# Optimization experiments

Measured on AMD Instinct MI355X. Metric: run time of the kernel, lower is better.

## Reference

```python
import jax, jax.numpy as jnp
import numpy as np

B, S, D = 8, 1024, 1152
H, HD = 16, 72  # num_heads, head_dim

def setup_inputs() -> dict:
    key = jax.random.key(0)
    ks = jax.random.split(key, 7)
    hidden_states = jax.random.normal(ks[0], (B, S, D), dtype=jnp.float32)
    cos = jax.random.uniform(ks[1], (S, HD), dtype=jnp.float32)
    sin = jax.random.uniform(ks[2], (S, HD), dtype=jnp.float32)
    qkv_w = jax.random.normal(ks[3], (3 * D, D), dtype=jnp.float32) * 0.02
    qkv_b = jnp.zeros((3 * D,), dtype=jnp.float32)
    proj_w = jax.random.normal(ks[4], (D, D), dtype=jnp.float32) * 0.02
    proj_b = jnp.zeros((D,), dtype=jnp.float32)
    return {"hidden_states": hidden_states, "cos": cos, "sin": sin,
            "qkv_w": qkv_w, "qkv_b": qkv_b, "proj_w": proj_w, "proj_b": proj_b}

def _rotate_half(x):
    x1, x2 = jnp.split(x, 2, axis=-1)
    return jnp.concatenate((-x2, x1), axis=-1)

def reference(hidden_states, cos, sin, qkv_w, qkv_b, proj_w, proj_b):
    b, s, d = hidden_states.shape
    # fused QKV projection
    qkv = hidden_states @ qkv_w.T + qkv_b            # [B,S,3D]
    qkv = qkv.reshape(b, s, 3, H, HD)
    qkv = jnp.transpose(qkv, (2, 0, 3, 1, 4))        # [3,B,H,S,HD]
    q, k, v = qkv[0], qkv[1], qkv[2]
    # rotary embedding, cos/sin broadcast [1,1,S,HD]
    c = cos[None, None, :, :]
    sn = sin[None, None, :, :]
    q = q * c + _rotate_half(q) * sn
    k = k * c + _rotate_half(k) * sn
    # SDPA
    scale = HD ** -0.5
    scores = jnp.einsum('bhqd,bhkd->bhqk', q, k) * scale
    probs = jax.nn.softmax(scores, axis=-1)
    attn = jnp.einsum('bhqk,bhkd->bhqd', probs, v)   # [B,H,S,HD]
    attn = jnp.transpose(attn, (0, 2, 1, 3)).reshape(b, s, d)
    return attn @ proj_w.T + proj_b
```

## Files before the change

### kernel.cpp

```cpp
#include <hip/hip_runtime.h>
#include <hip/hip_bf16.h>


typedef __attribute__((ext_vector_type(8))) short short8;
typedef __attribute__((ext_vector_type(4))) float f32x4;

__device__ __forceinline__ unsigned int f2bf(float f) {
    unsigned int u = __float_as_uint(f);
    return (u + 0x7FFFu + ((u >> 16) & 1u)) >> 16;
}

__device__ __forceinline__ void stout(float* C, size_t idx, float v) { C[idx] = v; }
__device__ __forceinline__ void stout(__hip_bfloat16* C, size_t idx, float v) {
    C[idx] = __float2bfloat16(v);
}

__device__ __forceinline__ void async_cp16(const void* g, void* l) {
    __builtin_amdgcn_global_load_lds((const __attribute__((address_space(1))) void*)g,
                                     (__attribute__((address_space(3))) void*)l, 16, 0, 0);
}

__global__ void f32_to_bf16_pair(
    const float* __restrict__ s0, unsigned short* __restrict__ d0, int n0_4,
    const float* __restrict__ s1, unsigned short* __restrict__ d1, int n1_4,
    unsigned short* __restrict__ dz, int nz_4)
{
    int i = blockIdx.x * 256 + threadIdx.x;
    if (i < n0_4) {
        float4 f = ((const float4*)s0)[i];
        ushort4 r;
        r.x = (unsigned short)f2bf(f.x);
        r.y = (unsigned short)f2bf(f.y);
        r.z = (unsigned short)f2bf(f.z);
        r.w = (unsigned short)f2bf(f.w);
        ((ushort4*)d0)[i] = r;
        return;
    }
    i -= n0_4;
    if (i < n1_4) {
        float4 f = ((const float4*)s1)[i];
        ushort4 r;
        r.x = (unsigned short)f2bf(f.x);
        r.y = (unsigned short)f2bf(f.y);
        r.z = (unsigned short)f2bf(f.z);
        r.w = (unsigned short)f2bf(f.w);
        ((ushort4*)d1)[i] = r;
        return;
    }
    i -= n1_4;
    if (i < nz_4) {
        ushort4 z; z.x = 0; z.y = 0; z.z = 0; z.w = 0;
        ((ushort4*)dz)[i] = z;
    }
}

template <int ISB, int H>
__device__ __forceinline__ void stage_ht(const unsigned short* __restrict__ g, int ldg,
                                         int k0, unsigned short* l, int w, int lane)
{
#pragma unroll
    for (int t = 0; t < 2; t++) {
        const int c  = w * 2 + t;
        const int r0 = ISB ? ((c >> 2) * 64 + H * 32 + (c & 3) * 8)
                           : ((c & 8) * 16 + H * 64 + (c & 7) * 8);
        const int rl = r0 + (lane >> 3);
        const int gg = (lane & 7) ^ (lane >> 3);
        async_cp16(g + (size_t)rl * ldg + k0 + gg * 8, l + r0 * 64);
    }
}

#define LDA(MH, SRC)                                                              \
    _Pragma("unroll") for (int mi = 0; mi < 4; ++mi) {                            \
        Af[mi][0] = *(const short8*)((SRC) + aRow + (MH) * 4096 + mi * 1024 + g0); \
        Af[mi][1] = *(const short8*)((SRC) + aRow + (MH) * 4096 + mi * 1024 + g1); \
    }

#define LDB(DST, NH, SRC)                                                         \
    _Pragma("unroll") for (int ni = 0; ni < 2; ++ni) {                            \
        DST[ni][0] = *(const short8*)((SRC) + bRow + (NH) * 2048 + ni * 1024 + g0); \
        DST[ni][1] = *(const short8*)((SRC) + bRow + (NH) * 2048 + ni * 1024 + g1); \
    }

#define MFMAS(MH, NH, PB)                                                         \
    __builtin_amdgcn_s_setprio(1);                                                \
    _Pragma("unroll") for (int mi = 0; mi < 4; ++mi)                              \
    _Pragma("unroll") for (int ni = 0; ni < 2; ++ni) {                            \
        acc[(MH) * 4 + mi][(NH) * 2 + ni] = __builtin_amdgcn_mfma_f32_16x16x32_bf16( \
            Af[mi][0], PB[ni][0], acc[(MH) * 4 + mi][(NH) * 2 + ni], 0, 0, 0);    \
        acc[(MH) * 4 + mi][(NH) * 2 + ni] = __builtin_amdgcn_mfma_f32_16x16x32_bf16( \
            Af[mi][1], PB[ni][1], acc[(MH) * 4 + mi][(NH) * 2 + ni], 0, 0, 0);    \
    }                                                                             \
    __builtin_amdgcn_s_setprio(0);

#define MIDBAR()                                                   \
    do {                                                           \
        __builtin_amdgcn_s_barrier();                              \
        asm volatile("s_waitcnt lgkmcnt(0)" ::: "memory");         \
        __builtin_amdgcn_sched_barrier(0);                         \
    } while (0)

#define ENDBAR()                                                   \
    do {                                                           \
        __builtin_amdgcn_s_barrier();                              \
        __builtin_amdgcn_sched_barrier(0);                         \
    } while (0)

template <typename OT>
__global__ __launch_bounds__(512, 2) void gemm_bt_256(
    const __hip_bfloat16* __restrict__ Abf,
    const __hip_bfloat16* __restrict__ Bbf,
    const float* __restrict__ bias,
    OT* __restrict__ C,
    int M, int Nreal, int K)
{
    __shared__ __align__(16) unsigned short smem[2][2][256 * 64];

    const int tid  = threadIdx.x;
    const int lane = tid & 63;
    const int w    = tid >> 6;
    const int wm   = w >> 2;
    const int wn   = w & 3;
    const int q    = lane >> 4;
    const int fr   = lane & 15;
    const int xr   = fr & 7;

    const int nwg = gridDim.x * gridDim.y;
    const int lin = blockIdx.y * gridDim.x + blockIdx.x;
    const int swz = (lin & 7) * (nwg >> 3) + (lin >> 3);
    const int bn  = (swz % gridDim.x) * 256;
    const int bm  = (swz / gridDim.x) * 256;

    const unsigned short* Ag = (const unsigned short*)Abf + (size_t)bm * K;
    const unsigned short* Bg = (const unsigned short*)Bbf + (size_t)bn * K;

    unsigned short* s00 = &smem[0][0][0];
    unsigned short* s01 = &smem[0][1][0];
    unsigned short* s10 = &smem[1][0][0];
    unsigned short* s11 = &smem[1][1][0];

    const int NT = K >> 6;
    const int NI = NT >> 1;

    const int aRow = (wm * 128 + fr) * 64;
    const int bRow = (wn * 64 + fr) * 64;
    const int g0   = ((0 * 4 + q) ^ xr) * 8;
    const int g1   = ((1 * 4 + q) ^ xr) * 8;

    f32x4 acc[8][4];
#pragma unroll
    for (int i = 0; i < 8; i++)
#pragma unroll
        for (int j = 0; j < 4; j++) acc[i][j] = (f32x4){0.f, 0.f, 0.f, 0.f};

    short8 Af[4][2], Bf0[2][2], Bf1[2][2];

    stage_ht<0, 0>(Ag, K, 0, s00, w, lane);
    stage_ht<0, 1>(Ag, K, 0, s00, w, lane);
    stage_ht<1, 0>(Bg, K, 0, s01, w, lane);
    stage_ht<1, 1>(Bg, K, 0, s01, w, lane);
    stage_ht<0, 0>(Ag, K, 64, s10, w, lane);
    stage_ht<1, 1>(Bg, K, 64, s10 + 16384, w, lane);
    stage_ht<0, 1>(Ag, K, 64, s10, w, lane);
    asm volatile("s_waitcnt vmcnt(6)" ::: "memory");
    ENDBAR();

#pragma unroll 1
    for (int i = 0; i < NI; i++) {
        const int k1 = (2 * i + 1) * 64;
        const int t2 = 2 * i + 2, t3 = 2 * i + 3;
        const int k2 = (t2 < NT ? t2 : NT - 1) * 64;
        const int k3 = (t3 < NT ? t3 : NT - 1) * 64;

        LDA(0, s00);
        LDB(Bf0, 0, s01);
        stage_ht<1, 0>(Bg, K, k1, s11, w, lane);
        asm volatile("s_waitcnt lgkmcnt(8)" ::: "memory");
        MIDBAR();
        MFMAS(0, 0, Bf0);
        ENDBAR();

        LDB(Bf1, 1, s01);
        stage_ht<0, 0>(Ag, K, k2, s00, w, lane);
        MIDBAR();
        MFMAS(0, 1, Bf1);
        ENDBAR();

        LDA(1, s00);
        stage_ht<1, 1>(Bg, K, k2, s01, w, lane);
        MIDBAR();
        MFMAS(1, 1, Bf1);
        ENDBAR();

        stage_ht<0, 1>(Ag, K, k2, s00, w, lane);
        asm volatile("s_waitcnt vmcnt(6)" ::: "memory");
        MIDBAR();
        MFMAS(1, 0, Bf0);
        ENDBAR();

        LDA(0, s10);
        LDB(Bf0, 0, s11);
        stage_ht<1, 0>(Bg, K, k2, s01, w, lane);
        asm volatile("s_waitcnt lgkmcnt(8)" ::: "memory");
        MIDBAR();
        MFMAS(0, 0, Bf0);
        ENDBAR();

        LDB(Bf1, 1, s11);
        stage_ht<0, 0>(Ag, K, k3, s10, w, lane);
        MIDBAR();
        MFMAS(0, 1, Bf1);
        ENDBAR();

        LDA(1, s10);
        stage_ht<1, 1>(Bg, K, k3, s11, w, lane);
        MIDBAR();
        MFMAS(1, 1, Bf1);
        ENDBAR();

        stage_ht<0, 1>(Ag, K, k3, s10, w, lane);
        asm volatile("s_waitcnt vmcnt(6)" ::: "memory");
        MIDBAR();
        MFMAS(1, 0, Bf0);
        ENDBAR();
    }

#pragma unroll
    for (int mf = 0; mf < 8; mf++) {
        const int row = bm + wm * 128 + mf * 16 + q * 4;
#pragma unroll
        for (int nf = 0; nf < 4; nf++) {
            const int col = bn + wn * 64 + nf * 16 + fr;
            if (col < Nreal) {
                const float bv = bias[col];
#pragma unroll
                for (int r = 0; r < 4; r++)
                    stout(C, (size_t)(row + r) * Nreal + col, acc[mf][nf][r] + bv);
            }
        }
    }
}

__global__ void rope_v_prep(
    const __hip_bfloat16* __restrict__ qkv,
    const float* __restrict__ cosp,
    const float* __restrict__ sinp,
    __hip_bfloat16* __restrict__ Qo,
    __hip_bfloat16* __restrict__ Ko,
    __hip_bfloat16* __restrict__ Vt)
{
    __shared__ __align__(16) unsigned short T[64 * 72];
    const int tid = threadIdx.x;
    const int bh = blockIdx.x >> 4;
    const int st = blockIdx.x & 15;
    const int b = bh >> 4, h = bh & 15;
    const size_t row0 = ((size_t)b * 1024 + st * 64) * 3456;

    const unsigned short* vsrc = (const unsigned short*)qkv + row0 + 2304 + h * 72;
#pragma unroll
    for (int k = 0; k < 3; k++) {
        const int c = tid + k * 256;
        if (c < 576) {
            const int s = c / 9, off = (c % 9) * 8;
            *(uint4*)&T[c * 8] = *(const uint4*)(vsrc + (size_t)s * 3456 + off);
        }
    }

    const unsigned short* qkvp = (const unsigned short*)qkv;
    const float QS = 0.17002324f;
#pragma unroll
    for (int k = 0; k < 9; k++) {
        const int p = tid + k * 256;
        const int sl = p / 36, i = p % 36;
        const int sg = st * 64 + sl;
        const size_t row = row0 + (size_t)sl * 3456;
        const int col = h * 72 + i;

        const float c1 = cosp[sg * 72 + i];
        const float c2 = cosp[sg * 72 + i + 36];
        const float s1 = sinp[sg * 72 + i];
        const float s2 = sinp[sg * 72 + i + 36];

        const float qa = __uint_as_float((unsigned int)qkvp[row + col] << 16);
        const float qb = __uint_as_float((unsigned int)qkvp[row + col + 36] << 16);
        const float ka = __uint_as_float((unsigned int)qkvp[row + 1152 + col] << 16);
        const float kb = __uint_as_float((unsigned int)qkvp[row + 1152 + col + 36] << 16);

        const size_t ob = ((size_t)bh * 1024 + sg) * 72 + i;
        ((unsigned short*)Qo)[ob]      = (unsigned short)f2bf((qa * c1 - qb * s1) * QS);
        ((unsigned short*)Qo)[ob + 36] = (unsigned short)f2bf((qb * c2 + qa * s2) * QS);
        ((unsigned short*)Ko)[ob]      = (unsigned short)f2bf(ka * c1 - kb * s1);
        ((unsigned short*)Ko)[ob + 36] = (unsigned short)f2bf(kb * c2 + ka * s2);
    }

    __syncthreads();

    unsigned short* dst = (unsigned short*)Vt + (size_t)(bh * 16 + st) * 72 * 64;
#pragma unroll
    for (int k = 0; k < 9; k++) {
        const int o = tid + k * 256;
        const int d = o >> 5;
        const int sl = (o & 31) * 2;
        ushort2 v;
        v.x = T[sl * 72 + d];
        v.y = T[(sl + 1) * 72 + d];
        *(ushort2*)&dst[d * 64 + sl] = v;
    }
}

__global__ __launch_bounds__(256, 4) void attn_mfma(
    const __hip_bfloat16* __restrict__ Q,
    const __hip_bfloat16* __restrict__ K,
    const __hip_bfloat16* __restrict__ Vt,
    __hip_bfloat16* __restrict__ O)
{
    __shared__ __align__(16) unsigned short Ks[64][72];
    __shared__ __align__(16) unsigned short Vs[80][72];
    __shared__ __align__(16) unsigned short Ps[4][32][72];

    const int tid  = threadIdx.x;
    const int lane = tid & 63;
    const int w    = tid >> 6;
    const int quad = lane >> 4;
    const int fr   = lane & 15;
    const int bh   = blockIdx.x & 127;
    const int qt   = blockIdx.x >> 7;
    const int qbase = qt * 128 + w * 32;

    const short8 z8 = (short8){0,0,0,0,0,0,0,0};

    for (int idx = tid; idx < 8 * 72; idx += 256)
        Vs[72 + idx / 72][idx % 72] = (idx < 72) ? (unsigned short)0x3F80 : (unsigned short)0;

    const unsigned short* qp = (const unsigned short*)Q + ((size_t)bh * 1024 + qbase + fr) * 72;
    short8 qf[2][3];
#pragma unroll
    for (int sub = 0; sub < 2; sub++) {
        const unsigned short* qs = qp + sub * 16 * 72;
        qf[sub][0] = *(const short8*)(qs + quad * 8);
        qf[sub][1] = *(const short8*)(qs + 32 + quad * 8);
        qf[sub][2] = (quad == 0) ? *(const short8*)(qs + 64) : z8;
    }

    f32x4 Oa[2][5];
#pragma unroll
    for (int sub = 0; sub < 2; sub++)
#pragma unroll
        for (int n = 0; n < 5; n++) Oa[sub][n] = (f32x4){0.f, 0.f, 0.f, 0.f};

    const unsigned short* kg0 = (const unsigned short*)K + (size_t)bh * 1024 * 72;
    const unsigned short* vg0 = (const unsigned short*)Vt + (size_t)bh * 16 * 72 * 64;

#pragma unroll 1
    for (int t = 0; t < 16; t++) {
        __syncthreads();
        const unsigned short* kg = kg0 + (size_t)t * 64 * 72;
        const unsigned short* vg = vg0 + (size_t)t * 72 * 64;
#pragma unroll
        for (int k = 0; k < 3; k++) {
            const int c = tid + k * 256;
            if (c < 576) {
                *(uint4*)&((unsigned short*)Ks)[c * 8] = *(const uint4*)(kg + c * 8);
                *(uint4*)&Vs[c >> 3][(c & 7) * 8] = *(const uint4*)(vg + c * 8);
            }
        }
        __syncthreads();

#pragma unroll
        for (int nt = 0; nt < 4; nt++) {
            short8 b0 = *(const short8*)&Ks[nt * 16 + fr][quad * 8];
            short8 b1 = *(const short8*)&Ks[nt * 16 + fr][32 + quad * 8];
            short8 b2 = (quad == 0) ? *(const short8*)&Ks[nt * 16 + fr][64] : z8;
            f32x4 s0 = (f32x4){0.f, 0.f, 0.f, 0.f};
            f32x4 s1 = (f32x4){0.f, 0.f, 0.f, 0.f};
            s0 = __builtin_amdgcn_mfma_f32_16x16x32_bf16(qf[0][0], b0, s0, 0, 0, 0);
            s1 = __builtin_amdgcn_mfma_f32_16x16x32_bf16(qf[1][0], b0, s1, 0, 0, 0);
            s0 = __builtin_amdgcn_mfma_f32_16x16x32_bf16(qf[0][1], b1, s0, 0, 0, 0);
            s1 = __builtin_amdgcn_mfma_f32_16x16x32_bf16(qf[1][1], b1, s1, 0, 0, 0);
            s0 = __builtin_amdgcn_mfma_f32_16x16x32_bf16(qf[0][2], b2, s0, 0, 0, 0);
            s1 = __builtin_amdgcn_mfma_f32_16x16x32_bf16(qf[1][2], b2, s1, 0, 0, 0);
#pragma unroll
            for (int r = 0; r < 4; r++) {
                Ps[w][quad * 4 + r][nt * 16 + fr]      = (unsigned short)f2bf(exp2f(s0[r]));
                Ps[w][16 + quad * 4 + r][nt * 16 + fr] = (unsigned short)f2bf(exp2f(s1[r]));
            }
        }

#pragma unroll
        for (int ks = 0; ks < 2; ks++) {
            short8 ap0 = *(const short8*)&Ps[w][fr][ks * 32 + quad * 8];
            short8 ap1 = *(const short8*)&Ps[w][16 + fr][ks * 32 + quad * 8];
#pragma unroll
            for (int n = 0; n < 5; n++) {
                short8 bv = *(const short8*)&Vs[n * 16 + fr][ks * 32 + quad * 8];
                Oa[0][n] = __builtin_amdgcn_mfma_f32_16x16x32_bf16(ap0, bv, Oa[0][n], 0, 0, 0);
                Oa[1][n] = __builtin_amdgcn_mfma_f32_16x16x32_bf16(ap1, bv, Oa[1][n], 0, 0, 0);
            }
        }
    }

    const int lsrc = (lane & 48) | 8;
    const int b = bh >> 4, h = bh & 15;
    unsigned short* ob = (unsigned short*)O;
#pragma unroll
    for (int sub = 0; sub < 2; sub++) {
        float inv[4];
#pragma unroll
        for (int r = 0; r < 4; r++)
            inv[r] = 1.f / __shfl(Oa[sub][4][r], lsrc, 64);
#pragma unroll
        for (int n = 0; n < 5; n++) {
            const int d = n * 16 + fr;
            if (d < 72) {
#pragma unroll
                for (int r = 0; r < 4; r++) {
                    const size_t idx =
                        ((size_t)b * 1024 + qbase + sub * 16 + quad * 4 + r) * 1152 + h * 72 + d;
                    ob[idx] = (unsigned short)f2bf(Oa[sub][n][r] * inv[r]);
                }
            }
        }
    }
}

extern "C" void kernel_launch(void* const* d_in, const int* in_sizes, int n_in,
                              void* d_out, int out_size, void* d_ws, size_t ws_size,
                              hipStream_t stream)
{
    const float* hs     = (const float*)d_in[0];
    const float* cosp   = (const float*)d_in[1];
    const float* sinp   = (const float*)d_in[2];
    const float* qkv_w  = (const float*)d_in[3];
    const float* qkv_b  = (const float*)d_in[4];
    const float* proj_w = (const float*)d_in[5];
    const float* proj_b = (const float*)d_in[6];
    float* out = (float*)d_out;

    char* ws = (char*)d_ws;
    __hip_bfloat16* qkv_buf = (__hip_bfloat16*)ws;
    __hip_bfloat16* Qb = (__hip_bfloat16*)(ws + 56623104);
    __hip_bfloat16* Kb = Qb + 9437184;
    __hip_bfloat16* Vt = Kb + 9437184;
    __hip_bfloat16* Ab = qkv_buf;

    unsigned short* hs_bf = (unsigned short*)Qb;
    unsigned short* qw_bf = (unsigned short*)Kb;
    unsigned short* pw_bf = (unsigned short*)Qb;

    f32_to_bf16_pair<<<13248, 256, 0, stream>>>(hs, hs_bf, 2359296,
                                                qkv_w, qw_bf, 995328,
                                                qw_bf + 3981312, 36864);
    gemm_bt_256<__hip_bfloat16>
        <<<dim3(14, 32), 512, 0, stream>>>((const __hip_bfloat16*)hs_bf,
                                           (const __hip_bfloat16*)qw_bf,
                                           qkv_b, qkv_buf, 8192, 3456, 1152);
    rope_v_prep<<<2048, 256, 0, stream>>>(qkv_buf, cosp, sinp, Qb, Kb, Vt);
    attn_mfma<<<1024, 256, 0, stream>>>(Qb, Kb, Vt, Ab);
    f32_to_bf16_pair<<<1440, 256, 0, stream>>>(proj_w, pw_bf, 331776,
                                               nullptr, nullptr, 0,
                                               pw_bf + 1327104, 36864);
    gemm_bt_256<float>
        <<<dim3(5, 32), 512, 0, stream>>>((const __hip_bfloat16*)Ab,
                                          (const __hip_bfloat16*)pw_bf,
                                          proj_b, out, 8192, 1152, 1152);
}
```

Baseline: 312.7 us.

## Read K/V fragments directly from global memory and vectorize RoPE prep

The attention kernel stops staging K and V tiles in shared memory. It loads MFMA operand fragments straight from global memory, which removes two barriers per tile, and K and Vt are padded to an 80-element stride. The ones/zero padding rows of V that feed the softmax-denominator trick are now written once by the prep kernel instead of per block. The RoPE prep is vectorized to 4-element loads and stores, and s_setprio is raised around MFMA sequences. The risk is that every wave now re-reads K/V from global/L2 instead of sharing one LDS copy per block, which raises memory traffic and latency exposure.

```diff
diff --git a/kernel.cpp b/kernel.cpp
--- a/kernel.cpp
+++ b/kernel.cpp
@@ -8,6 +8,9 @@
 __device__ __forceinline__ unsigned int f2bf(float f) {
     unsigned int u = __float_as_uint(f);
     return (u + 0x7FFFu + ((u >> 16) & 1u)) >> 16;
+}
+__device__ __forceinline__ float bf2f(unsigned short u) {
+    return __uint_as_float((unsigned int)u << 16);
 }
 
 __device__ __forceinline__ void stout(float* C, size_t idx, float v) { C[idx] = v; }
@@ -268,33 +271,54 @@
     const unsigned short* qkvp = (const unsigned short*)qkv;
     const float QS = 0.17002324f;
 #pragma unroll
-    for (int k = 0; k < 9; k++) {
-        const int p = tid + k * 256;
-        const int sl = p / 36, i = p % 36;
-        const int sg = st * 64 + sl;
-        const size_t row = row0 + (size_t)sl * 3456;
-        const int col = h * 72 + i;
-
-        const float c1 = cosp[sg * 72 + i];
-        const float c2 = cosp[sg * 72 + i + 36];
-        const float s1 = sinp[sg * 72 + i];
-        const float s2 = sinp[sg * 72 + i + 36];
-
-        const float qa = __uint_as_float((unsigned int)qkvp[row + col] << 16);
-        const float qb = __uint_as_float((unsigned int)qkvp[row + col + 36] << 16);
-        const float ka = __uint_as_float((unsigned int)qkvp[row + 1152 + col] << 16);
-        const float kb = __uint_as_float((unsigned int)qkvp[row + 1152 + col + 36] << 16);
-
-        const size_t ob = ((size_t)bh * 1024 + sg) * 72 + i;
-        ((unsigned short*)Qo)[ob]      = (unsigned short)f2bf((qa * c1 - qb * s1) * QS);
-        ((unsigned short*)Qo)[ob + 36] = (unsigned short)f2bf((qb * c2 + qa * s2) * QS);
-        ((unsigned short*)Ko)[ob]      = (unsigned short)f2bf(ka * c1 - kb * s1);
-        ((unsigned short*)Ko)[ob + 36] = (unsigned short)f2bf(kb * c2 + ka * s2);
+    for (int k = 0; k < 3; k++) {
+        const int idx = tid + k * 256;
+        if (idx < 576) {
+            const int sl = idx / 9, iq = idx % 9;
+            const int i0 = iq * 4;
+            const int sg = st * 64 + sl;
+            const unsigned short* qrow = qkvp + row0 + (size_t)sl * 3456 + h * 72 + i0;
+
+            ushort4 ql = *(const ushort4*)(qrow);
+            ushort4 qh = *(const ushort4*)(qrow + 36);
+            ushort4 kl = *(const ushort4*)(qrow + 1152);
+            ushort4 kh = *(const ushort4*)(qrow + 1188);
+            float4 cl = *(const float4*)(cosp + sg * 72 + i0);
+            float4 ch = *(const float4*)(cosp + sg * 72 + i0 + 36);
+            float4 nl = *(const float4*)(sinp + sg * 72 + i0);
+            float4 nh = *(const float4*)(sinp + sg * 72 + i0 + 36);
+
+            unsigned short qlv[4] = {ql.x, ql.y, ql.z, ql.w};
+            unsigned short qhv[4] = {qh.x, qh.y, qh.z, qh.w};
+            unsigned short klv[4] = {kl.x, kl.y, kl.z, kl.w};
+            unsigned short khv[4] = {kh.x, kh.y, kh.z, kh.w};
+            float clv[4] = {cl.x, cl.y, cl.z, cl.w};
+            float chv[4] = {ch.x, ch.y, ch.z, ch.w};
+            float nlv[4] = {nl.x, nl.y, nl.z, nl.w};
+            float nhv[4] = {nh.x, nh.y, nh.z, nh.w};
+
+            unsigned short qol[4], qoh[4], kol[4], koh[4];
+#pragma unroll
+            for (int j = 0; j < 4; j++) {
+                const float qa = bf2f(qlv[j]), qb = bf2f(qhv[j]);
+                const float ka = bf2f(klv[j]), kb = bf2f(khv[j]);
+                qol[j] = (unsigned short)f2bf((qa * clv[j] - qb * nlv[j]) * QS);
+                qoh[j] = (unsigned short)f2bf((qb * chv[j] + qa * nhv[j]) * QS);
+                kol[j] = (unsigned short)f2bf(ka * clv[j] - kb * nlv[j]);
+                koh[j] = (unsigned short)f2bf(kb * chv[j] + ka * nhv[j]);
+            }
+            unsigned short* qob = (unsigned short*)Qo + ((size_t)bh * 1024 + sg) * 72 + i0;
+            unsigned short* kob = (unsigned short*)Ko + ((size_t)bh * 1024 + sg) * 80 + i0;
+            *(ushort4*)qob        = (ushort4){qol[0], qol[1], qol[2], qol[3]};
+            *(ushort4*)(qob + 36) = (ushort4){qoh[0], qoh[1], qoh[2], qoh[3]};
+            *(ushort4*)kob        = (ushort4){kol[0], kol[1], kol[2], kol[3]};
+            *(ushort4*)(kob + 36) = (ushort4){koh[0], koh[1], koh[2], koh[3]};
+        }
     }
 
     __syncthreads();
 
-    unsigned short* dst = (unsigned short*)Vt + (size_t)(bh * 16 + st) * 72 * 64;
+    unsigned short* dst = (unsigned short*)Vt + (size_t)(bh * 16 + st) * 80 * 64;
 #pragma unroll
     for (int k = 0; k < 9; k++) {
         const int o = tid + k * 256;
@@ -305,6 +329,8 @@
         v.y = T[(sl + 1) * 72 + d];
         *(ushort2*)&dst[d * 64 + sl] = v;
     }
+    if (tid < 64) dst[72 * 64 + tid] = (unsigned short)0x3F80;
+    for (int z = tid; z < 7 * 64; z += 256) dst[73 * 64 + z] = 0;
 }
 
 __global__ __launch_bounds__(256, 4) void attn_mfma(
@@ -313,8 +339,6 @@
     const __hip_bfloat16* __restrict__ Vt,
     __hip_bfloat16* __restrict__ O)
 {
-    __shared__ __align__(16) unsigned short Ks[64][72];
-    __shared__ __align__(16) unsigned short Vs[80][72];
     __shared__ __align__(16) unsigned short Ps[4][32][72];
 
     const int tid  = threadIdx.x;
@@ -328,9 +352,6 @@
 
     const short8 z8 = (short8){0,0,0,0,0,0,0,0};
 
-    for (int idx = tid; idx < 8 * 72; idx += 256)
-        Vs[72 + idx / 72][idx % 72] = (idx < 72) ? (unsigned short)0x3F80 : (unsigned short)0;
-
     const unsigned short* qp = (const unsigned short*)Q + ((size_t)bh * 1024 + qbase + fr) * 72;
     short8 qf[2][3];
 #pragma unroll
@@ -347,37 +368,30 @@
 #pragma unroll
         for (int n = 0; n < 5; n++) Oa[sub][n] = (f32x4){0.f, 0.f, 0.f, 0.f};
 
-    const unsigned short* kg0 = (const unsigned short*)K + (size_t)bh * 1024 * 72;
-    const unsigned short* vg0 = (const unsigned short*)Vt + (size_t)bh * 16 * 72 * 64;
+    const unsigned short* kg0 = (const unsigned short*)K + (size_t)bh * 1024 * 80;
+    const unsigned short* vg0 = (const unsigned short*)Vt + (size_t)bh * 16 * 80 * 64;
 
 #pragma unroll 1
     for (int t = 0; t < 16; t++) {
-        __syncthreads();
-        const unsigned short* kg = kg0 + (size_t)t * 64 * 72;
-        const unsigned short* vg = vg0 + (size_t)t * 72 * 64;
-#pragma unroll
-        for (int k = 0; k < 3; k++) {
-            const int c = tid + k * 256;
-            if (c < 576) {
-                *(uint4*)&((unsigned short*)Ks)[c * 8] = *(const uint4*)(kg + c * 8);
-                *(uint4*)&Vs[c >> 3][(c & 7) * 8] = *(const uint4*)(vg + c * 8);
-            }
-        }
-        __syncthreads();
+        const unsigned short* kg = kg0 + (size_t)t * 64 * 80;
+        const unsigned short* vg = vg0 + (size_t)t * 80 * 64;
 
 #pragma unroll
         for (int nt = 0; nt < 4; nt++) {
-            short8 b0 = *(const short8*)&Ks[nt * 16 + fr][quad * 8];
-            short8 b1 = *(const short8*)&Ks[nt * 16 + fr][32 + quad * 8];
-            short8 b2 = (quad == 0) ? *(const short8*)&Ks[nt * 16 + fr][64] : z8;
+            const unsigned short* kr = kg + (nt * 16 + fr) * 80;
+            short8 b0 = *(const short8*)(kr + quad * 8);
+            short8 b1 = *(const short8*)(kr + 32 + quad * 8);
+            short8 b2 = (quad == 0) ? *(const short8*)(kr + 64) : z8;
             f32x4 s0 = (f32x4){0.f, 0.f, 0.f, 0.f};
             f32x4 s1 = (f32x4){0.f, 0.f, 0.f, 0.f};
+            __builtin_amdgcn_s_setprio(1);
             s0 = __builtin_amdgcn_mfma_f32_16x16x32_bf16(qf[0][0], b0, s0, 0, 0, 0);
             s1 = __builtin_amdgcn_mfma_f32_16x16x32_bf16(qf[1][0], b0, s1, 0, 0, 0);
             s0 = __builtin_amdgcn_mfma_f32_16x16x32_bf16(qf[0][1], b1, s0, 0, 0, 0);
             s1 = __builtin_amdgcn_mfma_f32_16x16x32_bf16(qf[1][1], b1, s1, 0, 0, 0);
             s0 = __builtin_amdgcn_mfma_f32_16x16x32_bf16(qf[0][2], b2, s0, 0, 0, 0);
             s1 = __builtin_amdgcn_mfma_f32_16x16x32_bf16(qf[1][2], b2, s1, 0, 0, 0);
+            __builtin_amdgcn_s_setprio(0);
 #pragma unroll
             for (int r = 0; r < 4; r++) {
                 Ps[w][quad * 4 + r][nt * 16 + fr]      = (unsigned short)f2bf(exp2f(s0[r]));
@@ -389,12 +403,17 @@
         for (int ks = 0; ks < 2; ks++) {
             short8 ap0 = *(const short8*)&Ps[w][fr][ks * 32 + quad * 8];
             short8 ap1 = *(const short8*)&Ps[w][16 + fr][ks * 32 + quad * 8];
+            short8 bv[5];
+#pragma unroll
+            for (int n = 0; n < 5; n++)
+                bv[n] = *(const short8*)(vg + (n * 16 + fr) * 64 + ks * 32 + quad * 8);
+            __builtin_amdgcn_s_setprio(1);
 #pragma unroll
             for (int n = 0; n < 5; n++) {
-                short8 bv = *(const short8*)&Vs[n * 16 + fr][ks * 32 + quad * 8];
-                Oa[0][n] = __builtin_amdgcn_mfma_f32_16x16x32_bf16(ap0, bv, Oa[0][n], 0, 0, 0);
-                Oa[1][n] = __builtin_amdgcn_mfma_f32_16x16x32_bf16(ap1, bv, Oa[1][n], 0, 0, 0);
+                Oa[0][n] = __builtin_amdgcn_mfma_f32_16x16x32_bf16(ap0, bv[n], Oa[0][n], 0, 0, 0);
+                Oa[1][n] = __builtin_amdgcn_mfma_f32_16x16x32_bf16(ap1, bv[n], Oa[1][n], 0, 0, 0);
             }
+            __builtin_amdgcn_s_setprio(0);
         }
     }
 
@@ -439,7 +458,7 @@
     __hip_bfloat16* qkv_buf = (__hip_bfloat16*)ws;
     __hip_bfloat16* Qb = (__hip_bfloat16*)(ws + 56623104);
     __hip_bfloat16* Kb = Qb + 9437184;
-    __hip_bfloat16* Vt = Kb + 9437184;
+    __hip_bfloat16* Vt = Kb + 10485760;
     __hip_bfloat16* Ab = qkv_buf;
 
     unsigned short* hs_bf = (unsigned short*)Qb;
```

Result: slower. 348.1 us (+11.3%).
